# Kernel tuning notes

Hardware: AMD Instinct MI355X
Metric: run time of the kernel (lower is better)

Reference implementation:

```python
import jax, jax.numpy as jnp
import numpy as np

N = 50000   # nodes
E = 600000  # edges
D = 128     # in_feats
H = 128     # n_hidden
C = 47      # n_classes


def setup_inputs() -> dict:
    key = jax.random.key(0)
    ks = jax.random.split(key, 12)
    x = jax.random.normal(ks[0], (N, D), dtype=jnp.float32)
    src = jax.random.randint(ks[1], (E,), 0, N, dtype=jnp.int32)
    dst = jax.random.randint(ks[2], (E,), 0, N, dtype=jnp.int32)
    def lin(k, fi, fo):
        s = 1.0 / np.sqrt(fi)
        return jax.random.uniform(k, (fi, fo), jnp.float32, -s, s)
    return {
        "x": x, "src": src, "dst": dst,
        "W_self0": lin(ks[3], D, H), "W_neigh0": lin(ks[4], D, H), "b0": jnp.zeros((H,), jnp.float32),
        "W_self1": lin(ks[5], H, H), "W_neigh1": lin(ks[6], H, H), "b1": jnp.zeros((H,), jnp.float32),
        "W_self2": lin(ks[7], H, C), "W_neigh2": lin(ks[8], H, C), "b2": jnp.zeros((C,), jnp.float32),
    }


def _sage_layer(h, src, dst, W_self, W_neigh, b, act):
    # gather neighbor (src) features, mean-aggregate onto dst nodes
    msum = jax.ops.segment_sum(h[src], dst, num_segments=N)           # [N, F]
    deg = jax.ops.segment_sum(jnp.ones((src.shape[0], 1), h.dtype), dst, num_segments=N)
    h_neigh = msum / jnp.maximum(deg, 1.0)                            # zero-degree -> 0
    out = h @ W_self + h_neigh @ W_neigh + b
    return jax.nn.relu(out) if act else out


def reference(x, src, dst, W_self0, W_neigh0, b0, W_self1, W_neigh1, b1, W_self2, W_neigh2, b2):
    h = _sage_layer(x, src, dst, W_self0, W_neigh0, b0, True)
    h = _sage_layer(h, src, dst, W_self1, W_neigh1, b1, True)
    h = _sage_layer(h, src, dst, W_self2, W_neigh2, b2, False)
    return h
```

## Files before the change

### kernel.cpp

```cpp
#include <hip/hip_runtime.h>
#include <hip/hip_bf16.h>


#define THREADS 256

typedef unsigned short u16;
typedef __attribute__((ext_vector_type(8))) short bf16x8;
typedef __attribute__((ext_vector_type(4))) float f32x4;

__device__ inline u16 f2bf(float f) {
    union { float f; unsigned u; } v; v.f = f;
    unsigned r = (v.u + 0x7FFFu + ((v.u >> 16) & 1u)) >> 16;
    return (u16)r;
}
__device__ inline float bf2f(u16 b) {
    union { unsigned u; float f; } v; v.u = ((unsigned)b) << 16;
    return v.f;
}
__device__ inline unsigned pack2(float a, float b) {
    return (unsigned)f2bf(a) | ((unsigned)f2bf(b) << 16);
}

#define GLDS16(gp, lp)                                                         \
    __builtin_amdgcn_global_load_lds(                                          \
        (const __attribute__((address_space(1))) void*)(gp),                   \
        (__attribute__((address_space(3))) void*)(lp), 16, 0, 0)

__global__ void k_preamble(const float* __restrict__ x, u16* __restrict__ hi,
                           u16* __restrict__ lo, int n32,
                           const int* __restrict__ dst, int* __restrict__ deg, int E,
                           const float* __restrict__ Ws0, const float* __restrict__ Wn0,
                           const float* __restrict__ Ws1, const float* __restrict__ Wn1,
                           const float* __restrict__ Ws2, const float* __restrict__ Wn2,
                           u16* __restrict__ Bt) {
    int idx = blockIdx.x * blockDim.x + threadIdx.x;
    if (idx < n32) {
        float4 v = ((const float4*)x)[idx];
        float h0 = bf2f(f2bf(v.x)), h1 = bf2f(f2bf(v.y)), h2 = bf2f(f2bf(v.z)), h3 = bf2f(f2bf(v.w));
        uint2 hp, lp;
        hp.x = pack2(h0, h1); hp.y = pack2(h2, h3);
        lp.x = pack2(v.x - h0, v.y - h1); lp.y = pack2(v.z - h2, v.w - h3);
        ((uint2*)hi)[idx] = hp;
        ((uint2*)lo)[idx] = lp;
    }
    if (idx < E) atomicAdd(&deg[dst[idx]], 1);
    if (idx < 3 * 128 * 256) {
        int layer = idx >> 15;
        int within = idx & 32767;
        int col = within >> 8;
        int k = within & 255;
        const float* Ws = (layer == 0) ? Ws0 : (layer == 1) ? Ws1 : Ws2;
        const float* Wn = (layer == 0) ? Wn0 : (layer == 1) ? Wn1 : Wn2;
        int fout = (layer == 2) ? 47 : 128;
        float v = 0.f;
        if (col < fout) v = (k < 128) ? Ws[k * fout + col] : Wn[(k - 128) * fout + col];
        u16 h = f2bf(v);
        Bt[layer * 65536 + within] = h;
        Bt[layer * 65536 + 32768 + within] = f2bf(v - bf2f(h));
    }
}

__global__ void k_scan_block(const int* __restrict__ deg, int* __restrict__ off,
                             int* __restrict__ bsum, int n) {
    __shared__ int s[256];
    int t = threadIdx.x;
    int base = blockIdx.x * 1024 + t * 4;
    int v[4];
#pragma unroll
    for (int i = 0; i < 4; i++) v[i] = (base + i < n) ? deg[base + i] : 0;
    int sum = v[0] + v[1] + v[2] + v[3];
    int val = sum;
    s[t] = val;
    __syncthreads();
    for (int o = 1; o < 256; o <<= 1) {
        int x = (t >= o) ? s[t - o] : 0;
        __syncthreads();
        val += x;
        s[t] = val;
        __syncthreads();
    }
    int run = val - sum;
#pragma unroll
    for (int i = 0; i < 4; i++) {
        if (base + i < n) off[base + i] = run;
        run += v[i];
    }
    if (t == 255) bsum[blockIdx.x] = val;
}

__global__ void k_scan_add(int* __restrict__ off, const int* __restrict__ bsum, int n) {
    __shared__ int sAdd;
    int t = threadIdx.x;
    if (t < 64) {
        int v = 0;
        for (int i = t; i < blockIdx.x; i += 64) v += bsum[i];
#pragma unroll
        for (int o = 32; o; o >>= 1) v += __shfl_xor(v, o, 64);
        if (t == 0) sAdd = v;
    }
    __syncthreads();
    int add = sAdd;
    int base = blockIdx.x * 1024 + t * 4;
#pragma unroll
    for (int i = 0; i < 4; i++)
        if (base + i < n) off[base + i] += add;
}

__global__ void k_fill(const int* __restrict__ src, const int* __restrict__ dst,
                       int* __restrict__ off, int* __restrict__ eidx, int E) {
    int e = blockIdx.x * blockDim.x + threadIdx.x;
    if (e < E) {
        int d = dst[e];
        int p = atomicAdd(&off[d], 1);
        eidx[p] = src[e];
    }
}

__global__ void k_aggregate(const u16* __restrict__ hi_in, const int* __restrict__ eidx,
                            const int* __restrict__ off, const int* __restrict__ deg,
                            u16* __restrict__ mhi, u16* __restrict__ mlo, int n) {
    int wv = blockIdx.x * 4 + (threadIdx.x >> 6);
    int lane = threadIdx.x & 63;
    int quarter = lane >> 4;
    int ql = lane & 15;
    int node = wv * 4 + quarter;
    if (node >= n) return;
    int cnt = deg[node];
    int base = off[node] - cnt;
    const uint4* h4 = (const uint4*)hi_in;
    float acc[8];
#pragma unroll
    for (int i = 0; i < 8; i++) acc[i] = 0.f;
    for (int j = 0; j < cnt; j += 8) {
        int s[8];
        float m[8];
#pragma unroll
        for (int u = 0; u < 8; u++) {
            int jj = j + u;
            s[u] = eidx[base + (jj < cnt ? jj : 0)];
            m[u] = (jj < cnt) ? 1.f : 0.f;
        }
        uint4 v[8];
#pragma unroll
        for (int u = 0; u < 8; u++) v[u] = h4[(size_t)s[u] * 16 + ql];
#pragma unroll
        for (int u = 0; u < 8; u++) {
            acc[0] = fmaf(m[u], bf2f((u16)(v[u].x & 0xffffu)), acc[0]);
            acc[1] = fmaf(m[u], bf2f((u16)(v[u].x >> 16)), acc[1]);
            acc[2] = fmaf(m[u], bf2f((u16)(v[u].y & 0xffffu)), acc[2]);
            acc[3] = fmaf(m[u], bf2f((u16)(v[u].y >> 16)), acc[3]);
            acc[4] = fmaf(m[u], bf2f((u16)(v[u].z & 0xffffu)), acc[4]);
            acc[5] = fmaf(m[u], bf2f((u16)(v[u].z >> 16)), acc[5]);
            acc[6] = fmaf(m[u], bf2f((u16)(v[u].w & 0xffffu)), acc[6]);
            acc[7] = fmaf(m[u], bf2f((u16)(v[u].w >> 16)), acc[7]);
        }
    }
    float iv = 1.0f / (float)(cnt > 1 ? cnt : 1);
    float a[8], r[8];
#pragma unroll
    for (int i = 0; i < 8; i++) {
        a[i] = acc[i] * iv;
        r[i] = bf2f(f2bf(a[i]));
    }
    uint4 hp, lp;
    hp.x = pack2(a[0], a[1]); hp.y = pack2(a[2], a[3]);
    hp.z = pack2(a[4], a[5]); hp.w = pack2(a[6], a[7]);
    lp.x = pack2(a[0] - r[0], a[1] - r[1]); lp.y = pack2(a[2] - r[2], a[3] - r[3]);
    lp.z = pack2(a[4] - r[4], a[5] - r[5]); lp.w = pack2(a[6] - r[6], a[7] - r[7]);
    ((uint4*)mhi)[(size_t)node * 16 + ql] = hp;
    ((uint4*)mlo)[(size_t)node * 16 + ql] = lp;
}

__global__ __launch_bounds__(256) void k_gemm_mfma(
    const u16* __restrict__ Ahi_s, const u16* __restrict__ Alo_s,
    const u16* __restrict__ Ahi_n, const u16* __restrict__ Alo_n,
    const u16* __restrict__ Bthi, const u16* __restrict__ Btlo,
    const float* __restrict__ bias, float* __restrict__ out_f32,
    u16* __restrict__ out_hi, u16* __restrict__ out_lo, int n, int fout, int relu) {
    __shared__ u16 sAhi[64 * 32];
    __shared__ u16 sAlo[64 * 32];
    __shared__ u16 sBhi[128 * 32];
    __shared__ u16 sBlo[128 * 32];

    int t = threadIdx.x;
    int w = t >> 6;
    int lane = t & 63;
    int wr = w >> 1, wc = w & 1;
    size_t row0 = (size_t)blockIdx.x * 64;

    const bool slim = (fout <= 64);
    const int rbase = slim ? (w * 16) : (wr * 32);
    const int nR = slim ? 1 : 2;
    const int cbase = slim ? 0 : (wc * 64);

    f32x4 acc[2][4];
#pragma unroll
    for (int r = 0; r < 2; r++)
#pragma unroll
        for (int c = 0; c < 4; c++) acc[r][c] = (f32x4){0.f, 0.f, 0.f, 0.f};

    int fr = lane & 15;
    int q = lane >> 4;

    for (int kk = 0; kk < 256; kk += 32) {
        const u16* Phi = (kk < 128) ? Ahi_s : Ahi_n;
        const u16* Plo = (kk < 128) ? Alo_s : Alo_n;
        int kc = kk & 127;
        __syncthreads();
        {
            int r = w * 16 + (lane >> 2);
            int s = lane & 3;
            int sg = s ^ ((r >> 1) & 3);
            GLDS16(Phi + (row0 + r) * 128 + kc + sg * 8, &sAhi[r * 32 + s * 8]);
            GLDS16(Plo + (row0 + r) * 128 + kc + sg * 8, &sAlo[r * 32 + s * 8]);
        }
#pragma unroll
        for (int i = 0; i < 2; i++) {
            int c = w * 32 + i * 16 + (lane >> 2);
            int s = lane & 3;
            int sg = s ^ ((c >> 1) & 3);
            GLDS16(Bthi + (size_t)c * 256 + kk + sg * 8, &sBhi[c * 32 + s * 8]);
            GLDS16(Btlo + (size_t)c * 256 + kk + sg * 8, &sBlo[c * 32 + s * 8]);
        }
        __syncthreads();

        bf16x8 a_hi[2], a_lo[2], b_hi[4], b_lo[4];
#pragma unroll
        for (int r = 0; r < 2; r++) {
            if (r >= nR) continue;
            int row = rbase + r * 16 + fr;
            int ad = row * 32 + ((q ^ ((row >> 1) & 3)) << 3);
            a_hi[r] = *(const bf16x8*)&sAhi[ad];
            a_lo[r] = *(const bf16x8*)&sAlo[ad];
        }
#pragma unroll
        for (int c = 0; c < 4; c++) {
            int col = cbase + c * 16 + fr;
            int ad = col * 32 + ((q ^ ((col >> 1) & 3)) << 3);
            b_hi[c] = *(const bf16x8*)&sBhi[ad];
            b_lo[c] = *(const bf16x8*)&sBlo[ad];
        }
#pragma unroll
        for (int r = 0; r < 2; r++) {
            if (r >= nR) continue;
#pragma unroll
            for (int c = 0; c < 4; c++) {
                acc[r][c] = __builtin_amdgcn_mfma_f32_16x16x32_bf16(
                    a_hi[r], b_hi[c], acc[r][c], 0, 0, 0);
                acc[r][c] = __builtin_amdgcn_mfma_f32_16x16x32_bf16(
                    a_hi[r], b_lo[c], acc[r][c], 0, 0, 0);
                acc[r][c] = __builtin_amdgcn_mfma_f32_16x16x32_bf16(
                    a_lo[r], b_hi[c], acc[r][c], 0, 0, 0);
            }
        }
    }

    int quad = lane >> 4;
    int lcol = lane & 15;
#pragma unroll
    for (int r = 0; r < 2; r++) {
        if (r >= nR) continue;
#pragma unroll
        for (int c = 0; c < 4; c++) {
            int col = cbase + c * 16 + lcol;
            float bv = (col < fout) ? bias[col] : 0.f;
#pragma unroll
            for (int g = 0; g < 4; g++) {
                size_t row = row0 + rbase + r * 16 + quad * 4 + g;
                if (row >= (size_t)n || col >= fout) continue;
                float v = acc[r][c][g] + bv;
                if (relu) v = v > 0.f ? v : 0.f;
                if (out_f32) out_f32[row * fout + col] = v;
                if (out_hi) {
                    u16 h = f2bf(v);
                    out_hi[row * 128 + col] = h;
                    out_lo[row * 128 + col] = f2bf(v - bf2f(h));
                }
            }
        }
    }
}

extern "C" void kernel_launch(void* const* d_in, const int* in_sizes, int n_in,
                              void* d_out, int out_size, void* d_ws, size_t ws_size,
                              hipStream_t stream) {
    const float* x = (const float*)d_in[0];
    const int* src = (const int*)d_in[1];
    const int* dst = (const int*)d_in[2];
    const float* Ws0 = (const float*)d_in[3];
    const float* Wn0 = (const float*)d_in[4];
    const float* b0 = (const float*)d_in[5];
    const float* Ws1 = (const float*)d_in[6];
    const float* Wn1 = (const float*)d_in[7];
    const float* b1 = (const float*)d_in[8];
    const float* Ws2 = (const float*)d_in[9];
    const float* Wn2 = (const float*)d_in[10];
    const float* b2 = (const float*)d_in[11];
    float* out = (float*)d_out;

    const int N = in_sizes[0] / 128;
    const int E = in_sizes[1];
    const int Npad = ((N + 63) / 64) * 64;

    char* p = (char*)d_ws;
    u16* P0hi = (u16*)p; p += (size_t)Npad * 128 * 2;
    u16* P0lo = (u16*)p; p += (size_t)Npad * 128 * 2;
    u16* P1hi = (u16*)p; p += (size_t)Npad * 128 * 2;
    u16* P1lo = (u16*)p; p += (size_t)Npad * 128 * 2;
    u16* Mhi = (u16*)p; p += (size_t)Npad * 128 * 2;
    u16* Mlo = (u16*)p; p += (size_t)Npad * 128 * 2;
    u16* Bt = (u16*)p; p += 3 * 2 * 128 * 256 * 2;
    int* deg = (int*)p; p += (size_t)N * 4;
    int* off = (int*)p; p += (size_t)N * 4;
    int* eidx = (int*)p; p += (size_t)E * 4;
    int* bsum = (int*)p;

    const int nPX = N * 32;
    int nPre = nPX;
    if (E > nPre) nPre = E;
    if (3 * 128 * 256 > nPre) nPre = 3 * 128 * 256;
    const int nbPre = (nPre + THREADS - 1) / THREADS;
    const int nbE = (E + THREADS - 1) / THREADS;
    const int nbScan = (N + 1023) / 1024;
    const int nbAgg = (N + 15) / 16;
    const int nbGemm = (N + 63) / 64;

    hipMemsetAsync(deg, 0, (size_t)N * sizeof(int), stream);

    k_preamble<<<nbPre, THREADS, 0, stream>>>(x, P0hi, P0lo, nPX, dst, deg, E,
                                              Ws0, Wn0, Ws1, Wn1, Ws2, Wn2, Bt);
    k_scan_block<<<nbScan, 256, 0, stream>>>(deg, off, bsum, N);
    k_scan_add<<<nbScan, 256, 0, stream>>>(off, bsum, N);
    k_fill<<<nbE, THREADS, 0, stream>>>(src, dst, off, eidx, E);

    k_aggregate<<<nbAgg, 256, 0, stream>>>(P0hi, eidx, off, deg, Mhi, Mlo, N);
    k_gemm_mfma<<<nbGemm, 256, 0, stream>>>(P0hi, P0lo, Mhi, Mlo,
                                            Bt + 0 * 65536, Bt + 0 * 65536 + 32768, b0,
                                            (float*)nullptr, P1hi, P1lo, N, 128, 1);
    k_aggregate<<<nbAgg, 256, 0, stream>>>(P1hi, eidx, off, deg, Mhi, Mlo, N);
    k_gemm_mfma<<<nbGemm, 256, 0, stream>>>(P1hi, P1lo, Mhi, Mlo,
                                            Bt + 1 * 65536, Bt + 1 * 65536 + 32768, b1,
                                            (float*)nullptr, P0hi, P0lo, N, 128, 1);
    k_aggregate<<<nbAgg, 256, 0, stream>>>(P0hi, eidx, off, deg, Mhi, Mlo, N);
    k_gemm_mfma<<<nbGemm, 256, 0, stream>>>(P0hi, P0lo, Mhi, Mlo,
                                            Bt + 2 * 65536, Bt + 2 * 65536 + 32768, b2,
                                            out, (u16*)nullptr, (u16*)nullptr, N, 47, 0);
}
```

Measured before the change: 299.2 us.

## Double-buffer GEMM LDS staging and skip unused column tile for slim output

The MFMA GEMM's shared-memory tiles are combined into one buffer with two stages. The next K-slice is now loaded with global_load_lds while the current slice is being multiplied, which drops one barrier per iteration and overlaps global loads with MFMA work. For the narrow last layer (fout<=64), the fourth 16-column tile is skipped in loads, MFMAs and the epilogue, since 47 columns fit in three tiles. This doubles LDS use per block, which may lower occupancy.

```diff
diff --git a/kernel.cpp b/kernel.cpp
--- a/kernel.cpp
+++ b/kernel.cpp
@@ -171,16 +171,19 @@
     ((uint4*)mlo)[(size_t)node * 16 + ql] = lp;
 }
 
+#define BUFO 12288
+#define AHI_O 0
+#define ALO_O 2048
+#define BHI_O 4096
+#define BLO_O 8192
+
 __global__ __launch_bounds__(256) void k_gemm_mfma(
     const u16* __restrict__ Ahi_s, const u16* __restrict__ Alo_s,
     const u16* __restrict__ Ahi_n, const u16* __restrict__ Alo_n,
     const u16* __restrict__ Bthi, const u16* __restrict__ Btlo,
     const float* __restrict__ bias, float* __restrict__ out_f32,
     u16* __restrict__ out_hi, u16* __restrict__ out_lo, int n, int fout, int relu) {
-    __shared__ u16 sAhi[64 * 32];
-    __shared__ u16 sAlo[64 * 32];
-    __shared__ u16 sBhi[128 * 32];
-    __shared__ u16 sBlo[128 * 32];
+    __shared__ u16 smem[2 * BUFO];
 
     int t = threadIdx.x;
     int w = t >> 6;
@@ -191,6 +194,7 @@
     const bool slim = (fout <= 64);
     const int rbase = slim ? (w * 16) : (wr * 32);
     const int nR = slim ? 1 : 2;
+    const int nC = slim ? 3 : 4;
     const int cbase = slim ? 0 : (wc * 64);
 
     f32x4 acc[2][4];
@@ -202,49 +206,63 @@
     int fr = lane & 15;
     int q = lane >> 4;
 
-    for (int kk = 0; kk < 256; kk += 32) {
-        const u16* Phi = (kk < 128) ? Ahi_s : Ahi_n;
-        const u16* Plo = (kk < 128) ? Alo_s : Alo_n;
-        int kc = kk & 127;
+    int sr = w * 16 + (lane >> 2);
+    int ss = lane & 3;
+    int sgA = ss ^ ((sr >> 1) & 3);
+    int sc0 = w * 32 + (lane >> 2);
+    int sc1 = sc0 + 16;
+    int sgB0 = ss ^ ((sc0 >> 1) & 3);
+    int sgB1 = ss ^ ((sc1 >> 1) & 3);
+
+#define STAGE(ks_, b_)                                                          \
+    {                                                                           \
+        int kk_ = (ks_) * 32;                                                   \
+        const u16* Phi_ = (kk_ < 128) ? Ahi_s : Ahi_n;                          \
+        const u16* Plo_ = (kk_ < 128) ? Alo_s : Alo_n;                          \
+        int kc_ = kk_ & 127;                                                    \
+        GLDS16(Phi_ + (row0 + sr) * 128 + kc_ + sgA * 8,                        \
+               &smem[(b_) * BUFO + AHI_O + sr * 32 + ss * 8]);                  \
+        GLDS16(Plo_ + (row0 + sr) * 128 + kc_ + sgA * 8,                        \
+               &smem[(b_) * BUFO + ALO_O + sr * 32 + ss * 8]);                  \
+        GLDS16(Bthi + (size_t)sc0 * 256 + kk_ + sgB0 * 8,                       \
+               &smem[(b_) * BUFO + BHI_O + sc0 * 32 + ss * 8]);                 \
+        GLDS16(Btlo + (size_t)sc0 * 256 + kk_ + sgB0 * 8,                       \
+               &smem[(b_) * BUFO + BLO_O + sc0 * 32 + ss * 8]);                 \
+        GLDS16(Bthi + (size_t)sc1 * 256 + kk_ + sgB1 * 8,                       \
+               &smem[(b_) * BUFO + BHI_O + sc1 * 32 + ss * 8]);                 \
+        GLDS16(Btlo + (size_t)sc1 * 256 + kk_ + sgB1 * 8,                       \
+               &smem[(b_) * BUFO + BLO_O + sc1 * 32 + ss * 8]);                 \
+    }
+
+    STAGE(0, 0);
+    for (int ks = 0; ks < 8; ks++) {
+        int b = ks & 1;
         __syncthreads();
-        {
-            int r = w * 16 + (lane >> 2);
-            int s = lane & 3;
-            int sg = s ^ ((r >> 1) & 3);
-            GLDS16(Phi + (row0 + r) * 128 + kc + sg * 8, &sAhi[r * 32 + s * 8]);
-            GLDS16(Plo + (row0 + r) * 128 + kc + sg * 8, &sAlo[r * 32 + s * 8]);
-        }
-#pragma unroll
-        for (int i = 0; i < 2; i++) {
-            int c = w * 32 + i * 16 + (lane >> 2);
-            int s = lane & 3;
-            int sg = s ^ ((c >> 1) & 3);
-            GLDS16(Bthi + (size_t)c * 256 + kk + sg * 8, &sBhi[c * 32 + s * 8]);
-            GLDS16(Btlo + (size_t)c * 256 + kk + sg * 8, &sBlo[c * 32 + s * 8]);
-        }
-        __syncthreads();
+        if (ks < 7) STAGE(ks + 1, b ^ 1);
 
         bf16x8 a_hi[2], a_lo[2], b_hi[4], b_lo[4];
 #pragma unroll
         for (int r = 0; r < 2; r++) {
             if (r >= nR) continue;
             int row = rbase + r * 16 + fr;
-            int ad = row * 32 + ((q ^ ((row >> 1) & 3)) << 3);
-            a_hi[r] = *(const bf16x8*)&sAhi[ad];
-            a_lo[r] = *(const bf16x8*)&sAlo[ad];
+            int ad = b * BUFO + row * 32 + ((q ^ ((row >> 1) & 3)) << 3);
+            a_hi[r] = *(const bf16x8*)&smem[AHI_O + ad];
+            a_lo[r] = *(const bf16x8*)&smem[ALO_O + ad];
         }
 #pragma unroll
         for (int c = 0; c < 4; c++) {
+            if (c >= nC) continue;
             int col = cbase + c * 16 + fr;
-            int ad = col * 32 + ((q ^ ((col >> 1) & 3)) << 3);
-            b_hi[c] = *(const bf16x8*)&sBhi[ad];
-            b_lo[c] = *(const bf16x8*)&sBlo[ad];
+            int ad = b * BUFO + col * 32 + ((q ^ ((col >> 1) & 3)) << 3);
+            b_hi[c] = *(const bf16x8*)&smem[BHI_O + ad];
+            b_lo[c] = *(const bf16x8*)&smem[BLO_O + ad];
         }
 #pragma unroll
         for (int r = 0; r < 2; r++) {
             if (r >= nR) continue;
 #pragma unroll
             for (int c = 0; c < 4; c++) {
+                if (c >= nC) continue;
                 acc[r][c] = __builtin_amdgcn_mfma_f32_16x16x32_bf16(
                     a_hi[r], b_hi[c], acc[r][c], 0, 0, 0);
                 acc[r][c] = __builtin_amdgcn_mfma_f32_16x16x32_bf16(
@@ -254,6 +272,7 @@
             }
         }
     }
+#undef STAGE
 
     int quad = lane >> 4;
     int lcol = lane & 15;
@@ -262,6 +281,7 @@
         if (r >= nR) continue;
 #pragma unroll
         for (int c = 0; c < 4; c++) {
+            if (c >= nC) continue;
             int col = cbase + c * 16 + lcol;
             float bv = (col < fout) ? bias[col] : 0.f;
 #pragma unroll
```

Result: slower. 308.5 us (+3.1%).
